# Optimization experiments

Hardware: AMD Instinct MI355X
Metric: run time of the kernel (lower is better)

## Reference

```python
import jax, jax.numpy as jnp
import numpy as np

B, T_MAX = 512, 200
FEAT, HID, MLP_HID, OUT = 256, 1024, 1024, 256


def _uniform(k, shape, fan_in):
    lim = 1.0 / np.sqrt(fan_in)
    return jax.random.uniform(k, shape, jnp.float32, -lim, lim)


def setup_inputs() -> dict:
    key = jax.random.key(0)
    ks = jax.random.split(key, 20)
    # lengths: sorted descending (packed-sequence convention), in [T_MAX//2, T_MAX]
    rng = np.random.RandomState(0)
    lengths = np.sort(rng.randint(T_MAX // 2, T_MAX + 1, size=B))[::-1].copy()
    inp = {
        "features": jax.random.normal(ks[0], (B, FEAT), jnp.float32),
        "lengths": jnp.asarray(lengths, jnp.int32),
        # pre-drawn reparameterization noise for the emission sampler, one per step
        "eps": jax.random.normal(ks[1], (T_MAX, B, OUT), jnp.float32),
        # feature2hidden Linear(feature_size, rnn_hidden_size)
        "W_f2h": _uniform(ks[2], (HID, FEAT), FEAT),
        "b_f2h": jnp.zeros((HID,), jnp.float32),
        # GRUCell(OUT, HID)
        "W_ih": _uniform(ks[3], (3 * HID, OUT), HID),
        "b_ih": _uniform(ks[4], (3 * HID,), HID),
        "W_hh": _uniform(ks[5], (3 * HID, HID), HID),
        "b_hh": _uniform(ks[6], (3 * HID,), HID),
        # MLP1 (emission param 1): Linear(HID, MLP_HID) -> tanh -> Linear(MLP_HID, OUT)
        "W1a": _uniform(ks[7], (MLP_HID, HID), HID), "b1a": jnp.zeros((MLP_HID,), jnp.float32),
        "W1b": _uniform(ks[8], (OUT, MLP_HID), MLP_HID), "b1b": jnp.zeros((OUT,), jnp.float32),
        # MLP2 (emission param 2)
        "W2a": _uniform(ks[9], (MLP_HID, HID), HID), "b2a": jnp.zeros((MLP_HID,), jnp.float32),
        "W2b": _uniform(ks[10], (OUT, MLP_HID), MLP_HID), "b2b": jnp.zeros((OUT,), jnp.float32),
        # offset_predictor Linear(HID, 2)  (computed then discarded in the original)
        "W_off": _uniform(ks[11], (2, HID), HID), "b_off": jnp.zeros((2,), jnp.float32),
    }
    return inp


def _packed_indices(lengths_np, T):
    # batch_sizes[t] = number of sequences with length > t (lengths sorted descending)
    bs = (lengths_np[None, :] > np.arange(T)[:, None]).sum(axis=1)
    t_idx = np.repeat(np.arange(T), bs)
    b_idx = np.concatenate([np.arange(b) for b in bs])
    return jnp.asarray(t_idx), jnp.asarray(b_idx)


def reference(features, lengths, eps, W_f2h, b_f2h, W_ih, b_ih, W_hh, b_hh,
              W1a, b1a, W1b, b1b, W2a, b2a, W2b, b2b, W_off, b_off):
    lengths_np = np.asarray(lengths)
    T = int(lengths_np.max())
    Bsz = features.shape[0]
    Dout = W_ih.shape[1]

    # (reshape_hidden returns None and init_hidden is never passed to the cell).
    _dead = features @ W_f2h.T + b_f2h

    gh_r, gh_z, gh_n = jnp.split(b_hh, 3)  # h_prev == 0 every step -> W_hh @ 0 drops out

    def mlp(h, Wa, ba, Wb, bb):
        return jnp.tanh(h @ Wa.T + ba) @ Wb.T + bb

    def step(x, eps_t):
        gi = x @ W_ih.T + b_ih                      # [B, 3H]
        gi_r, gi_z, gi_n = jnp.split(gi, 3, axis=-1)
        r = jax.nn.sigmoid(gi_r + gh_r)
        z = jax.nn.sigmoid(gi_z + gh_z)
        n = jnp.tanh(gi_n + r * gh_n)
        h = (1.0 - z) * n                           # GRUCell with zero init hidden
        p1 = mlp(h, W1a, b1a, W1b, b1b)             # emission param 1 (loc)
        p2 = mlp(h, W2a, b2a, W2b, b2b)             # emission param 2 (log-var)
        x_next = p1 + jnp.exp(0.5 * p2) * eps_t     # reparameterized Gaussian sample
        return x_next, (h, p1, p2)

    x0 = jnp.zeros((Bsz, Dout), features.dtype)
    _, (hs, p1s, p2s) = jax.lax.scan(step, x0, eps[:T])  # each [T, B, .]

    t_idx, b_idx = _packed_indices(lengths_np, T)
    flat_h = hs[t_idx, b_idx]     # [N, HID], N = sum(lengths)
    flat_p1 = p1s[t_idx, b_idx]   # [N, OUT]
    flat_p2 = p2s[t_idx, b_idx]   # [N, OUT]

    # offset predictor is computed but discarded by the original return statement
    _off = flat_h @ W_off.T + b_off

    return (flat_p1, flat_p2, flat_h)
```

## Files before the change

kernel.cpp:

```cpp
#include <hip/hip_runtime.h>
#include <math.h>

#define TMAX 200
#define CB   64

__device__ __forceinline__ float sig_(float x){ return 1.0f/(1.0f+expf(-x)); }

__device__ __forceinline__ void cl_sync(int* cnt, int* go, int nblk, int ep, int tid)
{
    __syncthreads();
    if (tid == 0) {
        __threadfence();
        int old = __hip_atomic_fetch_add(cnt, 1, __ATOMIC_ACQ_REL, __HIP_MEMORY_SCOPE_AGENT);
        if (old == nblk - 1) {
            __hip_atomic_store(cnt, 0, __ATOMIC_RELAXED, __HIP_MEMORY_SCOPE_AGENT);
            __hip_atomic_store(go, ep, __ATOMIC_RELEASE, __HIP_MEMORY_SCOPE_AGENT);
        } else {
            while (__hip_atomic_load(go, __ATOMIC_ACQUIRE, __HIP_MEMORY_SCOPE_AGENT) < ep)
                __builtin_amdgcn_s_sleep(16);
        }
        __threadfence();
    }
    __syncthreads();
}

#define LDSF 11264

__global__ __launch_bounds__(256, 2)
void kfused(const int* __restrict__ lengths,
            const float* __restrict__ eps,
            const float* __restrict__ W_ih, const float* __restrict__ b_ih,
            const float* __restrict__ b_hh,
            const float* __restrict__ W1a, const float* __restrict__ b1a,
            const float* __restrict__ W1b, const float* __restrict__ b1b,
            const float* __restrict__ W2a, const float* __restrict__ b2a,
            const float* __restrict__ W2b, const float* __restrict__ b2b,
            float* __restrict__ out_p1, float* __restrict__ out_p2, float* __restrict__ out_h,
            int* __restrict__ bar, float* __restrict__ xT, float* __restrict__ hT,
            float* __restrict__ haT, int nblk)
{
    __shared__ float lds[LDSF];
    __shared__ int sbs[TMAX], soff[TMAX];

    const int tid = threadIdx.x;
    const int bid = blockIdx.x;
    const int cl  = bid & 7;
    const int r   = bid >> 3;
    const int cb  = cl * CB;

    int* cnt = &bar[cl * 64];
    int* go  = &bar[cl * 64 + 16];

    if (tid < TMAX) {
        int c = 0;
        for (int b = 0; b < 512; ++b) c += (lengths[b] > tid) ? 1 : 0;
        sbs[tid] = c;
    }
    __syncthreads();
    if (tid == 0) { int a = 0; for (int i = 0; i < TMAX; ++i) { soff[i] = a; a += sbs[i]; } }
    __syncthreads();

    for (int t = 0; t < TMAX; ++t) {
        const int bsz = sbs[t], ofs = soff[t];

        for (int s = r; s < 32; s += nblk) {
            const int j0 = s * 32;
            const int tx = tid & 15, ty = tid >> 4;
            float acc[4][6];
            #pragma unroll
            for (int i = 0; i < 4; ++i)
                #pragma unroll
                for (int q = 0; q < 6; ++q) acc[i][q] = 0.f;

            if (t > 0) {
                const int sk = tid >> 3, sb = (tid & 7) * 8;
                const int wj = tid >> 3, wk = (tid & 7) * 4;
                float4 px0, px1, pw0, pw1, pw2;
                px0 = *(const float4*)&xT[(size_t)sk * 512 + cb + sb];
                px1 = *(const float4*)&xT[(size_t)sk * 512 + cb + sb + 4];
                pw0 = *(const float4*)&W_ih[(size_t)(j0 + wj) * 256 + wk];
                pw1 = *(const float4*)&W_ih[(size_t)(1024 + j0 + wj) * 256 + wk];
                pw2 = *(const float4*)&W_ih[(size_t)(2048 + j0 + wj) * 256 + wk];
                {
                    float* xs = lds; float* ws = lds + 4864;
                    *(float4*)&xs[sk * 76 + sb] = px0;
                    *(float4*)&xs[sk * 76 + sb + 4] = px1;
                    const float* a0 = &pw0.x; const float* a1 = &pw1.x; const float* a2 = &pw2.x;
                    #pragma unroll
                    for (int m = 0; m < 4; ++m) {
                        ws[(wk+m)*100 + wj]      = a0[m];
                        ws[(wk+m)*100 + 32 + wj] = a1[m];
                        ws[(wk+m)*100 + 64 + wj] = a2[m];
                    }
                }
                for (int kc = 0; kc < 8; ++kc) {
                    __syncthreads();
                    const int cur = kc & 1;
                    if (kc < 7) {
                        const int kb = (kc + 1) * 32;
                        px0 = *(const float4*)&xT[(size_t)(kb + sk) * 512 + cb + sb];
                        px1 = *(const float4*)&xT[(size_t)(kb + sk) * 512 + cb + sb + 4];
                        pw0 = *(const float4*)&W_ih[(size_t)(j0 + wj) * 256 + kb + wk];
                        pw1 = *(const float4*)&W_ih[(size_t)(1024 + j0 + wj) * 256 + kb + wk];
                        pw2 = *(const float4*)&W_ih[(size_t)(2048 + j0 + wj) * 256 + kb + wk];
                    }
                    const float* xs = lds + cur * 2432;
                    const float* ws = lds + 4864 + cur * 3200;
                    #pragma unroll 4
                    for (int kk = 0; kk < 32; ++kk) {
                        const float4 a4 = *(const float4*)&xs[kk * 76 + ty * 4];
                        float w[6];
                        #pragma unroll
                        for (int q = 0; q < 6; ++q) w[q] = ws[kk * 100 + tx * 6 + q];
                        const float av[4] = {a4.x, a4.y, a4.z, a4.w};
                        #pragma unroll
                        for (int i = 0; i < 4; ++i)
                            #pragma unroll
                            for (int q = 0; q < 6; ++q)
                                acc[i][q] = fmaf(av[i], w[q], acc[i][q]);
                    }
                    if (kc < 7) {
                        float* xs2 = lds + (cur ^ 1) * 2432;
                        float* ws2 = lds + 4864 + (cur ^ 1) * 3200;
                        *(float4*)&xs2[sk * 76 + sb] = px0;
                        *(float4*)&xs2[sk * 76 + sb + 4] = px1;
                        const float* a0 = &pw0.x; const float* a1 = &pw1.x; const float* a2 = &pw2.x;
                        #pragma unroll
                        for (int m = 0; m < 4; ++m) {
                            ws2[(wk+m)*100 + wj]      = a0[m];
                            ws2[(wk+m)*100 + 32 + wj] = a1[m];
                            ws2[(wk+m)*100 + 64 + wj] = a2[m];
                        }
                    }
                }
            }
            __syncthreads();
            #pragma unroll
            for (int q = 0; q < 6; ++q) {
                const int n = tx * 6 + q;
                #pragma unroll
                for (int i = 0; i < 4; ++i) lds[n * 68 + ty * 4 + i] = acc[i][q];
            }
            __syncthreads();
            {
                const int jr = tid & 31, bq = (tid >> 5) * 8;
                const int j = j0 + jr;
                const float brr = b_ih[j] + b_hh[j];
                const float bzz = b_ih[1024 + j] + b_hh[1024 + j];
                const float bnn = b_ih[2048 + j];
                const float gnn = b_hh[2048 + j];
                float hv[8];
                #pragma unroll
                for (int i = 0; i < 8; ++i) {
                    const int b = bq + i;
                    const float rr = sig_(lds[jr * 68 + b] + brr);
                    const float zz = sig_(lds[(32 + jr) * 68 + b] + bzz);
                    const float nn = tanhf(lds[(64 + jr) * 68 + b] + bnn + rr * gnn);
                    hv[i] = (1.f - zz) * nn;
                    hT[(size_t)j * 512 + cb + b] = hv[i];
                }
                #pragma unroll
                for (int i = 0; i < 8; ++i) lds[6528 + jr * 68 + bq + i] = hv[i];
            }
            __syncthreads();
            {
                const int b = tid >> 2, q = tid & 3;
                if (cb + b < bsz) {
                    float4 v0, v1;
                    v0.x = lds[6528 + (q*8+0)*68 + b]; v0.y = lds[6528 + (q*8+1)*68 + b];
                    v0.z = lds[6528 + (q*8+2)*68 + b]; v0.w = lds[6528 + (q*8+3)*68 + b];
                    v1.x = lds[6528 + (q*8+4)*68 + b]; v1.y = lds[6528 + (q*8+5)*68 + b];
                    v1.z = lds[6528 + (q*8+6)*68 + b]; v1.w = lds[6528 + (q*8+7)*68 + b];
                    *(float4*)&out_h[(size_t)(ofs + cb + b) * 1024 + j0 + q * 8] = v0;
                    *(float4*)&out_h[(size_t)(ofs + cb + b) * 1024 + j0 + q * 8 + 4] = v1;
                }
            }
            __syncthreads();
        }
        cl_sync(cnt, go, nblk, t * 3 + 1, tid);

        for (int s = r; s < 32; s += nblk) {
            const int n0 = s * 64;
            const float* __restrict__ Wa = (n0 < 1024) ? W1a : W2a;
            const float* __restrict__ ba = (n0 < 1024) ? b1a : b2a;
            const int nr0 = n0 & 1023;
            const int tx = tid & 15, ty = tid >> 4;
            const int sk = tid >> 3, sb = (tid & 7) * 8;
            const int wn = tid >> 2, wk0 = (tid & 3) * 8;
            float acc[4][4];
            #pragma unroll
            for (int i = 0; i < 4; ++i)
                #pragma unroll
                for (int j = 0; j < 4; ++j) acc[i][j] = 0.f;

            float4 px0, px1, pw0, pw1;
            px0 = *(const float4*)&hT[(size_t)sk * 512 + cb + sb];
            px1 = *(const float4*)&hT[(size_t)sk * 512 + cb + sb + 4];
            pw0 = *(const float4*)&Wa[(size_t)(nr0 + wn) * 1024 + wk0];
            pw1 = *(const float4*)&Wa[(size_t)(nr0 + wn) * 1024 + wk0 + 4];
            {
                float* xs = lds; float* ws = lds + 4864;
                *(float4*)&xs[sk * 76 + sb] = px0;
                *(float4*)&xs[sk * 76 + sb + 4] = px1;
                const float* a0 = &pw0.x; const float* a1 = &pw1.x;
                #pragma unroll
                for (int m = 0; m < 4; ++m) {
                    ws[(wk0+m)*68 + wn]   = a0[m];
                    ws[(wk0+4+m)*68 + wn] = a1[m];
                }
            }
            for (int kc = 0; kc < 32; ++kc) {
                __syncthreads();
                const int cur = kc & 1;
                if (kc < 31) {
                    const int kb = (kc + 1) * 32;
                    px0 = *(const float4*)&hT[(size_t)(kb + sk) * 512 + cb + sb];
                    px1 = *(const float4*)&hT[(size_t)(kb + sk) * 512 + cb + sb + 4];
                    pw0 = *(const float4*)&Wa[(size_t)(nr0 + wn) * 1024 + kb + wk0];
                    pw1 = *(const float4*)&Wa[(size_t)(nr0 + wn) * 1024 + kb + wk0 + 4];
                }
                const float* xs = lds + cur * 2432;
                const float* ws = lds + 4864 + cur * 3200;
                #pragma unroll 4
                for (int kk = 0; kk < 32; ++kk) {
                    const float4 a4 = *(const float4*)&xs[kk * 76 + ty * 4];
                    const float4 w4 = *(const float4*)&ws[kk * 68 + tx * 4];
                    const float av[4] = {a4.x, a4.y, a4.z, a4.w};
                    const float wv[4] = {w4.x, w4.y, w4.z, w4.w};
                    #pragma unroll
                    for (int i = 0; i < 4; ++i)
                        #pragma unroll
                        for (int j = 0; j < 4; ++j)
                            acc[i][j] = fmaf(av[i], wv[j], acc[i][j]);
                }
                if (kc < 31) {
                    float* xs2 = lds + (cur ^ 1) * 2432;
                    float* ws2 = lds + 4864 + (cur ^ 1) * 3200;
                    *(float4*)&xs2[sk * 76 + sb] = px0;
                    *(float4*)&xs2[sk * 76 + sb + 4] = px1;
                    const float* a0 = &pw0.x; const float* a1 = &pw1.x;
                    #pragma unroll
                    for (int m = 0; m < 4; ++m) {
                        ws2[(wk0+m)*68 + wn]   = a0[m];
                        ws2[(wk0+4+m)*68 + wn] = a1[m];
                    }
                }
            }
            #pragma unroll
            for (int j = 0; j < 4; ++j) {
                const float bias = ba[nr0 + tx * 4 + j];
                float4 hv;
                hv.x = tanhf(acc[0][j] + bias);
                hv.y = tanhf(acc[1][j] + bias);
                hv.z = tanhf(acc[2][j] + bias);
                hv.w = tanhf(acc[3][j] + bias);
                *(float4*)&haT[(size_t)(n0 + tx * 4 + j) * 512 + cb + ty * 4] = hv;
            }
            __syncthreads();
        }
        cl_sync(cnt, go, nblk, t * 3 + 2, tid);

        for (int s = r; s < 32; s += nblk) {
            const int c0 = s * 8;
            const int g = tid >> 6, b = tid & 63;
            const int sk = tid >> 3, sb = (tid & 7) * 8;
            float accf[2][8];
            #pragma unroll
            for (int f = 0; f < 2; ++f)
                #pragma unroll
                for (int c = 0; c < 8; ++c) accf[f][c] = 0.f;

            #pragma unroll 1
            for (int f = 0; f < 2; ++f) {
                const float* __restrict__ Wb = f ? W2b : W1b;
                const float* __restrict__ hap = haT + (size_t)f * 1024 * 512;
                float4 px0, px1, pwv;
                px0 = *(const float4*)&hap[(size_t)sk * 512 + cb + sb];
                px1 = *(const float4*)&hap[(size_t)sk * 512 + cb + sb + 4];
                const int cw = (tid & 63) >> 3, ck = (tid & 7) * 4;
                if (tid < 64) pwv = *(const float4*)&Wb[(size_t)(c0 + cw) * 1024 + ck];
                {
                    float* xs = lds; float* ws = lds + 4864;
                    *(float4*)&xs[sk * 76 + sb] = px0;
                    *(float4*)&xs[sk * 76 + sb + 4] = px1;
                    if (tid < 64) {
                        const float* a0 = &pwv.x;
                        #pragma unroll
                        for (int m = 0; m < 4; ++m) ws[(ck+m)*12 + cw] = a0[m];
                    }
                }
                for (int kc = 0; kc < 32; ++kc) {
                    __syncthreads();
                    const int cur = kc & 1;
                    if (kc < 31) {
                        const int kb = (kc + 1) * 32;
                        px0 = *(const float4*)&hap[(size_t)(kb + sk) * 512 + cb + sb];
                        px1 = *(const float4*)&hap[(size_t)(kb + sk) * 512 + cb + sb + 4];
                        if (tid < 64) pwv = *(const float4*)&Wb[(size_t)(c0 + cw) * 1024 + kb + ck];
                    }
                    const float* xs = lds + cur * 2432;
                    const float* ws = lds + 4864 + cur * 3200;
                    #pragma unroll
                    for (int k8 = 0; k8 < 8; ++k8) {
                        const int kk = g * 8 + k8;
                        const float a = xs[kk * 76 + b];
                        const float4 wlo = *(const float4*)&ws[kk * 12];
                        const float4 whi = *(const float4*)&ws[kk * 12 + 4];
                        accf[f][0] = fmaf(a, wlo.x, accf[f][0]);
                        accf[f][1] = fmaf(a, wlo.y, accf[f][1]);
                        accf[f][2] = fmaf(a, wlo.z, accf[f][2]);
                        accf[f][3] = fmaf(a, wlo.w, accf[f][3]);
                        accf[f][4] = fmaf(a, whi.x, accf[f][4]);
                        accf[f][5] = fmaf(a, whi.y, accf[f][5]);
                        accf[f][6] = fmaf(a, whi.z, accf[f][6]);
                        accf[f][7] = fmaf(a, whi.w, accf[f][7]);
                    }
                    if (kc < 31) {
                        float* xs2 = lds + (cur ^ 1) * 2432;
                        float* ws2 = lds + 4864 + (cur ^ 1) * 3200;
                        *(float4*)&xs2[sk * 76 + sb] = px0;
                        *(float4*)&xs2[sk * 76 + sb + 4] = px1;
                        if (tid < 64) {
                            const float* a0 = &pwv.x;
                            #pragma unroll
                            for (int m = 0; m < 4; ++m) ws2[(ck+m)*12 + cw] = a0[m];
                        }
                    }
                }
            }
            __syncthreads();
            #pragma unroll
            for (int c = 0; c < 8; ++c) {
                lds[((0 * 4 + g) * 8 + c) * 68 + b] = accf[0][c];
                lds[((1 * 4 + g) * 8 + c) * 68 + b] = accf[1][c];
            }
            {
                const int b2 = tid >> 2, q = tid & 3;
                const float2 e = *(const float2*)&eps[(size_t)t * 131072 + (size_t)(cb + b2) * 256 + c0 + q * 2];
                lds[4864 + b2 * 12 + q * 2]     = e.x;
                lds[4864 + b2 * 12 + q * 2 + 1] = e.y;
            }
            __syncthreads();
            {
                const int cp = tid >> 6;
                #pragma unroll
                for (int e = 0; e < 2; ++e) {
                    const int cc = cp * 2 + e;
                    float p1 = b1b[c0 + cc], p2 = b2b[c0 + cc];
                    #pragma unroll
                    for (int gg = 0; gg < 4; ++gg) {
                        p1 += lds[((0 * 4 + gg) * 8 + cc) * 68 + b];
                        p2 += lds[((1 * 4 + gg) * 8 + cc) * 68 + b];
                    }
                    const float x = fmaf(expf(0.5f * p2), lds[4864 + b * 12 + cc], p1);
                    xT[(size_t)(c0 + cc) * 512 + cb + b] = x;
                    lds[5700 + b * 20 + cc]     = p1;
                    lds[5700 + b * 20 + 8 + cc] = p2;
                }
            }
            __syncthreads();
            {
                const int bb2 = tid >> 2, q = tid & 3;
                if (cb + bb2 < bsz) {
                    if (q < 2) {
                        *(float4*)&out_p1[(size_t)(ofs + cb + bb2) * 256 + c0 + q * 4] =
                            *(const float4*)&lds[5700 + bb2 * 20 + q * 4];
                    } else {
                        *(float4*)&out_p2[(size_t)(ofs + cb + bb2) * 256 + c0 + (q - 2) * 4] =
                            *(const float4*)&lds[5700 + bb2 * 20 + 8 + (q - 2) * 4];
                    }
                }
            }
            __syncthreads();
        }
        cl_sync(cnt, go, nblk, t * 3 + 3, tid);
    }
}

extern "C" void kernel_launch(void* const* d_in, const int* in_sizes, int n_in,
                              void* d_out, int out_size, void* d_ws, size_t ws_size,
                              hipStream_t stream)
{
    (void)in_sizes; (void)n_in; (void)ws_size;
    const int*   lengths = (const int*)  d_in[1];
    const float* eps     = (const float*)d_in[2];
    const float* W_ih    = (const float*)d_in[5];
    const float* b_ih    = (const float*)d_in[6];
    const float* b_hh    = (const float*)d_in[8];
    const float* W1a     = (const float*)d_in[9];
    const float* b1a     = (const float*)d_in[10];
    const float* W1b     = (const float*)d_in[11];
    const float* b1b     = (const float*)d_in[12];
    const float* W2a     = (const float*)d_in[13];
    const float* b2a     = (const float*)d_in[14];
    const float* W2b     = (const float*)d_in[15];
    const float* b2b     = (const float*)d_in[16];

    float* out = (float*)d_out;
    const size_t N = (size_t)out_size / 1536;
    float* out_p1 = out;
    float* out_p2 = out + N * 256;
    float* out_h  = out + N * 512;

    int*   bar = (int*)d_ws;
    float* xT  = (float*)((char*)d_ws + 4096);
    float* hT  = xT + 131072;
    float* haT = hT + 524288;

    hipMemsetAsync(d_ws, 0, 4096, stream);

    int dev = 0;
    (void)hipGetDevice(&dev);
    int ncu = 0;
    if (hipDeviceGetAttribute(&ncu, hipDeviceAttributeMultiprocessorCount, dev) != hipSuccess || ncu <= 0)
        ncu = 256;
    int maxB = 0;
    if (hipOccupancyMaxActiveBlocksPerMultiprocessor(&maxB, (const void*)kfused, 256, 0) != hipSuccess || maxB <= 0)
        maxB = 1;
    long cap = (long)maxB * (long)ncu;
    int grd = (cap < 256) ? (int)(cap & ~7L) : 256;
    if (grd < 8) grd = 8;

    for (;;) {
        int nblk = grd >> 3;
        void* args[] = {
            (void*)&lengths, (void*)&eps, (void*)&W_ih, (void*)&b_ih, (void*)&b_hh,
            (void*)&W1a, (void*)&b1a, (void*)&W1b, (void*)&b1b,
            (void*)&W2a, (void*)&b2a, (void*)&W2b, (void*)&b2b,
            (void*)&out_p1, (void*)&out_p2, (void*)&out_h,
            (void*)&bar, (void*)&xT, (void*)&hT, (void*)&haT, (void*)&nblk
        };
        hipError_t err = hipLaunchCooperativeKernel((void*)kfused, dim3(grd), dim3(256), args, 0, stream);
        if (err == hipSuccess || grd <= 8) break;
        grd = (grd >> 1) & ~7;
        if (grd < 8) grd = 8;
    }
}
```

Measured before the change: 42.38 ms.

## Split batch into 16 clusters of 32 and shrink per-block tiles

Changes the cooperative decomposition from 8 batch clusters of 64 columns to 16 clusters of 32, doubling the grid to up to 512 blocks. Every GEMM tile, LDS layout and epilogue is rescaled to the 32-wide batch slice, and the MLP hidden stage is split into 64 tiles of 32 outputs. hT and haT writes are restaged through LDS so they go out as coalesced float4 stores. The aim is more blocks in flight per step and smaller per-cluster barrier groups. The cost is smaller register tiles with lower arithmetic intensity per LDS load, more blocks re-reading the weights, and the extra LDS staging passes.

```diff
diff --git a/kernel.cpp b/kernel.cpp
--- a/kernel.cpp
+++ b/kernel.cpp
@@ -2,7 +2,8 @@
 #include <math.h>
 
 #define TMAX 200
-#define CB   64
+#define NCL  16
+#define CB   32
 
 __device__ __forceinline__ float sig_(float x){ return 1.0f/(1.0f+expf(-x)); }
 
@@ -24,7 +25,7 @@
     __syncthreads();
 }
 
-#define LDSF 11264
+#define LDSF 8704
 
 __global__ __launch_bounds__(256, 2)
 void kfused(const int* __restrict__ lengths,
@@ -44,12 +45,12 @@
 
     const int tid = threadIdx.x;
     const int bid = blockIdx.x;
-    const int cl  = bid & 7;
-    const int r   = bid >> 3;
+    const int cl  = bid & 15;
+    const int r   = bid >> 4;
     const int cb  = cl * CB;
 
-    int* cnt = &bar[cl * 64];
-    int* go  = &bar[cl * 64 + 16];
+    int* cnt = &bar[cl * 16];
+    int* go  = &bar[cl * 16 + 8];
 
     if (tid < TMAX) {
         int c = 0;
@@ -66,25 +67,23 @@
         for (int s = r; s < 32; s += nblk) {
             const int j0 = s * 32;
             const int tx = tid & 15, ty = tid >> 4;
-            float acc[4][6];
+            float acc[2][6];
             #pragma unroll
-            for (int i = 0; i < 4; ++i)
+            for (int i = 0; i < 2; ++i)
                 #pragma unroll
                 for (int q = 0; q < 6; ++q) acc[i][q] = 0.f;
 
             if (t > 0) {
-                const int sk = tid >> 3, sb = (tid & 7) * 8;
+                const int sk = tid >> 3, sb = (tid & 7) * 4;
                 const int wj = tid >> 3, wk = (tid & 7) * 4;
-                float4 px0, px1, pw0, pw1, pw2;
-                px0 = *(const float4*)&xT[(size_t)sk * 512 + cb + sb];
-                px1 = *(const float4*)&xT[(size_t)sk * 512 + cb + sb + 4];
+                float4 px, pw0, pw1, pw2;
+                px  = *(const float4*)&xT[(size_t)sk * 512 + cb + sb];
                 pw0 = *(const float4*)&W_ih[(size_t)(j0 + wj) * 256 + wk];
                 pw1 = *(const float4*)&W_ih[(size_t)(1024 + j0 + wj) * 256 + wk];
                 pw2 = *(const float4*)&W_ih[(size_t)(2048 + j0 + wj) * 256 + wk];
                 {
-                    float* xs = lds; float* ws = lds + 4864;
-                    *(float4*)&xs[sk * 76 + sb] = px0;
-                    *(float4*)&xs[sk * 76 + sb + 4] = px1;
+                    float* xs = lds; float* ws = lds + 2304;
+                    *(float4*)&xs[sk * 36 + sb] = px;
                     const float* a0 = &pw0.x; const float* a1 = &pw1.x; const float* a2 = &pw2.x;
                     #pragma unroll
                     for (int m = 0; m < 4; ++m) {
@@ -98,32 +97,28 @@
                     const int cur = kc & 1;
                     if (kc < 7) {
                         const int kb = (kc + 1) * 32;
-                        px0 = *(const float4*)&xT[(size_t)(kb + sk) * 512 + cb + sb];
-                        px1 = *(const float4*)&xT[(size_t)(kb + sk) * 512 + cb + sb + 4];
+                        px  = *(const float4*)&xT[(size_t)(kb + sk) * 512 + cb + sb];
                         pw0 = *(const float4*)&W_ih[(size_t)(j0 + wj) * 256 + kb + wk];
                         pw1 = *(const float4*)&W_ih[(size_t)(1024 + j0 + wj) * 256 + kb + wk];
                         pw2 = *(const float4*)&W_ih[(size_t)(2048 + j0 + wj) * 256 + kb + wk];
                     }
-                    const float* xs = lds + cur * 2432;
-                    const float* ws = lds + 4864 + cur * 3200;
+                    const float* xs = lds + cur * 1152;
+                    const float* ws = lds + 2304 + cur * 3200;
                     #pragma unroll 4
                     for (int kk = 0; kk < 32; ++kk) {
-                        const float4 a4 = *(const float4*)&xs[kk * 76 + ty * 4];
-                        float w[6];
+                        const float a0v = xs[kk*36 + ty*2];
+                        const float a1v = xs[kk*36 + ty*2 + 1];
                         #pragma unroll
-                        for (int q = 0; q < 6; ++q) w[q] = ws[kk * 100 + tx * 6 + q];
-                        const float av[4] = {a4.x, a4.y, a4.z, a4.w};
-                        #pragma unroll
-                        for (int i = 0; i < 4; ++i)
-                            #pragma unroll
-                            for (int q = 0; q < 6; ++q)
-                                acc[i][q] = fmaf(av[i], w[q], acc[i][q]);
+                        for (int q = 0; q < 6; ++q) {
+                            const float w = ws[kk*100 + tx*6 + q];
+                            acc[0][q] = fmaf(a0v, w, acc[0][q]);
+                            acc[1][q] = fmaf(a1v, w, acc[1][q]);
+                        }
                     }
                     if (kc < 7) {
-                        float* xs2 = lds + (cur ^ 1) * 2432;
-                        float* ws2 = lds + 4864 + (cur ^ 1) * 3200;
-                        *(float4*)&xs2[sk * 76 + sb] = px0;
-                        *(float4*)&xs2[sk * 76 + sb + 4] = px1;
+                        float* xs2 = lds + (cur ^ 1) * 1152;
+                        float* ws2 = lds + 2304 + (cur ^ 1) * 3200;
+                        *(float4*)&xs2[sk * 36 + sb] = px;
                         const float* a0 = &pw0.x; const float* a1 = &pw1.x; const float* a2 = &pw2.x;
                         #pragma unroll
                         for (int m = 0; m < 4; ++m) {
@@ -138,123 +133,109 @@
             #pragma unroll
             for (int q = 0; q < 6; ++q) {
                 const int n = tx * 6 + q;
-                #pragma unroll
-                for (int i = 0; i < 4; ++i) lds[n * 68 + ty * 4 + i] = acc[i][q];
-            }
-            __syncthreads();
-            {
-                const int jr = tid & 31, bq = (tid >> 5) * 8;
+                lds[n*33 + ty*2]     = acc[0][q];
+                lds[n*33 + ty*2 + 1] = acc[1][q];
+            }
+            __syncthreads();
+            {
+                const int jr = tid & 31, bq = (tid >> 5) * 4;
                 const int j = j0 + jr;
                 const float brr = b_ih[j] + b_hh[j];
                 const float bzz = b_ih[1024 + j] + b_hh[1024 + j];
                 const float bnn = b_ih[2048 + j];
                 const float gnn = b_hh[2048 + j];
-                float hv[8];
-                #pragma unroll
-                for (int i = 0; i < 8; ++i) {
+                #pragma unroll
+                for (int i = 0; i < 4; ++i) {
                     const int b = bq + i;
-                    const float rr = sig_(lds[jr * 68 + b] + brr);
-                    const float zz = sig_(lds[(32 + jr) * 68 + b] + bzz);
-                    const float nn = tanhf(lds[(64 + jr) * 68 + b] + bnn + rr * gnn);
-                    hv[i] = (1.f - zz) * nn;
-                    hT[(size_t)j * 512 + cb + b] = hv[i];
-                }
-                #pragma unroll
-                for (int i = 0; i < 8; ++i) lds[6528 + jr * 68 + bq + i] = hv[i];
-            }
-            __syncthreads();
-            {
-                const int b = tid >> 2, q = tid & 3;
+                    const float rr = sig_(lds[jr*33 + b] + brr);
+                    const float zz = sig_(lds[(32+jr)*33 + b] + bzz);
+                    const float nn = tanhf(lds[(64+jr)*33 + b] + bnn + rr * gnn);
+                    lds[4096 + jr*33 + b] = (1.f - zz) * nn;
+                }
+            }
+            __syncthreads();
+            {
+                const int jj = tid >> 3, bq = (tid & 7) * 4;
+                float4 v = { lds[4096 + jj*33 + bq],     lds[4096 + jj*33 + bq + 1],
+                             lds[4096 + jj*33 + bq + 2], lds[4096 + jj*33 + bq + 3] };
+                *(float4*)&hT[(size_t)(j0 + jj) * 512 + cb + bq] = v;
+            }
+            {
+                const int b = tid >> 3, q = tid & 7;
                 if (cb + b < bsz) {
-                    float4 v0, v1;
-                    v0.x = lds[6528 + (q*8+0)*68 + b]; v0.y = lds[6528 + (q*8+1)*68 + b];
-                    v0.z = lds[6528 + (q*8+2)*68 + b]; v0.w = lds[6528 + (q*8+3)*68 + b];
-                    v1.x = lds[6528 + (q*8+4)*68 + b]; v1.y = lds[6528 + (q*8+5)*68 + b];
-                    v1.z = lds[6528 + (q*8+6)*68 + b]; v1.w = lds[6528 + (q*8+7)*68 + b];
-                    *(float4*)&out_h[(size_t)(ofs + cb + b) * 1024 + j0 + q * 8] = v0;
-                    *(float4*)&out_h[(size_t)(ofs + cb + b) * 1024 + j0 + q * 8 + 4] = v1;
+                    float4 v = { lds[4096 + (q*4+0)*33 + b], lds[4096 + (q*4+1)*33 + b],
+                                 lds[4096 + (q*4+2)*33 + b], lds[4096 + (q*4+3)*33 + b] };
+                    *(float4*)&out_h[(size_t)(ofs + cb + b) * 1024 + j0 + q*4] = v;
                 }
             }
             __syncthreads();
         }
         cl_sync(cnt, go, nblk, t * 3 + 1, tid);
 
-        for (int s = r; s < 32; s += nblk) {
-            const int n0 = s * 64;
+        for (int s = r; s < 64; s += nblk) {
+            const int n0 = s * 32;
             const float* __restrict__ Wa = (n0 < 1024) ? W1a : W2a;
             const float* __restrict__ ba = (n0 < 1024) ? b1a : b2a;
             const int nr0 = n0 & 1023;
             const int tx = tid & 15, ty = tid >> 4;
-            const int sk = tid >> 3, sb = (tid & 7) * 8;
-            const int wn = tid >> 2, wk0 = (tid & 3) * 8;
-            float acc[4][4];
-            #pragma unroll
-            for (int i = 0; i < 4; ++i)
-                #pragma unroll
-                for (int j = 0; j < 4; ++j) acc[i][j] = 0.f;
-
-            float4 px0, px1, pw0, pw1;
-            px0 = *(const float4*)&hT[(size_t)sk * 512 + cb + sb];
-            px1 = *(const float4*)&hT[(size_t)sk * 512 + cb + sb + 4];
-            pw0 = *(const float4*)&Wa[(size_t)(nr0 + wn) * 1024 + wk0];
-            pw1 = *(const float4*)&Wa[(size_t)(nr0 + wn) * 1024 + wk0 + 4];
-            {
-                float* xs = lds; float* ws = lds + 4864;
-                *(float4*)&xs[sk * 76 + sb] = px0;
-                *(float4*)&xs[sk * 76 + sb + 4] = px1;
-                const float* a0 = &pw0.x; const float* a1 = &pw1.x;
-                #pragma unroll
-                for (int m = 0; m < 4; ++m) {
-                    ws[(wk0+m)*68 + wn]   = a0[m];
-                    ws[(wk0+4+m)*68 + wn] = a1[m];
-                }
+            const int sk = tid >> 3, sb = (tid & 7) * 4;
+            const int wn = tid >> 3, wk0 = (tid & 7) * 4;
+            float acc[2][2] = {{0.f,0.f},{0.f,0.f}};
+
+            float4 px, pw;
+            px = *(const float4*)&hT[(size_t)sk * 512 + cb + sb];
+            pw = *(const float4*)&Wa[(size_t)(nr0 + wn) * 1024 + wk0];
+            {
+                float* xs = lds; float* ws = lds + 2304;
+                *(float4*)&xs[sk * 36 + sb] = px;
+                const float* a0 = &pw.x;
+                #pragma unroll
+                for (int m = 0; m < 4; ++m) ws[(wk0+m)*36 + wn] = a0[m];
             }
             for (int kc = 0; kc < 32; ++kc) {
                 __syncthreads();
                 const int cur = kc & 1;
                 if (kc < 31) {
                     const int kb = (kc + 1) * 32;
-                    px0 = *(const float4*)&hT[(size_t)(kb + sk) * 512 + cb + sb];
-                    px1 = *(const float4*)&hT[(size_t)(kb + sk) * 512 + cb + sb + 4];
-                    pw0 = *(const float4*)&Wa[(size_t)(nr0 + wn) * 1024 + kb + wk0];
-                    pw1 = *(const float4*)&Wa[(size_t)(nr0 + wn) * 1024 + kb + wk0 + 4];
-                }
-                const float* xs = lds + cur * 2432;
-                const float* ws = lds + 4864 + cur * 3200;
-                #pragma unroll 4
+                    px = *(const float4*)&hT[(size_t)(kb + sk) * 512 + cb + sb];
+                    pw = *(const float4*)&Wa[(size_t)(nr0 + wn) * 1024 + kb + wk0];
+                }
+                const float* xs = lds + cur * 1152;
+                const float* ws = lds + 2304 + cur * 1152;
+                #pragma unroll 8
                 for (int kk = 0; kk < 32; ++kk) {
-                    const float4 a4 = *(const float4*)&xs[kk * 76 + ty * 4];
-                    const float4 w4 = *(const float4*)&ws[kk * 68 + tx * 4];
-                    const float av[4] = {a4.x, a4.y, a4.z, a4.w};
-                    const float wv[4] = {w4.x, w4.y, w4.z, w4.w};
+                    const float a0v = xs[kk*36 + ty*2];
+                    const float a1v = xs[kk*36 + ty*2 + 1];
+                    const float w0 = ws[kk*36 + tx*2];
+                    const float w1 = ws[kk*36 + tx*2 + 1];
+                    acc[0][0] = fmaf(a0v, w0, acc[0][0]);
+                    acc[0][1] = fmaf(a0v, w1, acc[0][1]);
+                    acc[1][0] = fmaf(a1v, w0, acc[1][0]);
+                    acc[1][1] = fmaf(a1v, w1, acc[1][1]);
+                }
+                if (kc < 31) {
+                    float* xs2 = lds + (cur ^ 1) * 1152;
+                    float* ws2 = lds + 2304 + (cur ^ 1) * 1152;
+                    *(float4*)&xs2[sk * 36 + sb] = px;
+                    const float* a0 = &pw.x;
                     #pragma unroll
-                    for (int i = 0; i < 4; ++i)
-                        #pragma unroll
-                        for (int j = 0; j < 4; ++j)
-                            acc[i][j] = fmaf(av[i], wv[j], acc[i][j]);
-                }
-                if (kc < 31) {
-                    float* xs2 = lds + (cur ^ 1) * 2432;
-                    float* ws2 = lds + 4864 + (cur ^ 1) * 3200;
-                    *(float4*)&xs2[sk * 76 + sb] = px0;
-                    *(float4*)&xs2[sk * 76 + sb + 4] = px1;
-                    const float* a0 = &pw0.x; const float* a1 = &pw1.x;
-                    #pragma unroll
-                    for (int m = 0; m < 4; ++m) {
-                        ws2[(wk0+m)*68 + wn]   = a0[m];
-                        ws2[(wk0+4+m)*68 + wn] = a1[m];
-                    }
-                }
-            }
+                    for (int m = 0; m < 4; ++m) ws2[(wk0+m)*36 + wn] = a0[m];
+                }
+            }
+            __syncthreads();
             #pragma unroll
-            for (int j = 0; j < 4; ++j) {
-                const float bias = ba[nr0 + tx * 4 + j];
-                float4 hv;
-                hv.x = tanhf(acc[0][j] + bias);
-                hv.y = tanhf(acc[1][j] + bias);
-                hv.z = tanhf(acc[2][j] + bias);
-                hv.w = tanhf(acc[3][j] + bias);
-                *(float4*)&haT[(size_t)(n0 + tx * 4 + j) * 512 + cb + ty * 4] = hv;
+            for (int q = 0; q < 2; ++q) {
+                const int n = tx * 2 + q;
+                const float bias = ba[nr0 + n];
+                lds[n*33 + ty*2]     = tanhf(acc[0][q] + bias);
+                lds[n*33 + ty*2 + 1] = tanhf(acc[1][q] + bias);
+            }
+            __syncthreads();
+            {
+                const int nn = tid >> 3, bq = (tid & 7) * 4;
+                float4 v = { lds[nn*33 + bq],     lds[nn*33 + bq + 1],
+                             lds[nn*33 + bq + 2], lds[nn*33 + bq + 3] };
+                *(float4*)&haT[(size_t)(n0 + nn) * 512 + cb + bq] = v;
             }
             __syncthreads();
         }
@@ -262,8 +243,9 @@
 
         for (int s = r; s < 32; s += nblk) {
             const int c0 = s * 8;
-            const int g = tid >> 6, b = tid & 63;
-            const int sk = tid >> 3, sb = (tid & 7) * 8;
+            const int b = tid & 31, g = tid >> 5;
+            const int sk = tid >> 3, sb = (tid & 7) * 4;
+            const int cw = (tid & 63) >> 3, ck = (tid & 7) * 4;
             float accf[2][8];
             #pragma unroll
             for (int f = 0; f < 2; ++f)
@@ -274,17 +256,14 @@
             for (int f = 0; f < 2; ++f) {
                 const float* __restrict__ Wb = f ? W2b : W1b;
                 const float* __restrict__ hap = haT + (size_t)f * 1024 * 512;
-                float4 px0, px1, pwv;
-                px0 = *(const float4*)&hap[(size_t)sk * 512 + cb + sb];
-                px1 = *(const float4*)&hap[(size_t)sk * 512 + cb + sb + 4];
-                const int cw = (tid & 63) >> 3, ck = (tid & 7) * 4;
-                if (tid < 64) pwv = *(const float4*)&Wb[(size_t)(c0 + cw) * 1024 + ck];
+                float4 px, pw;
+                px = *(const float4*)&hap[(size_t)sk * 512 + cb + sb];
+                if (tid < 64) pw = *(const float4*)&Wb[(size_t)(c0 + cw) * 1024 + ck];
                 {
-                    float* xs = lds; float* ws = lds + 4864;
-                    *(float4*)&xs[sk * 76 + sb] = px0;
-                    *(float4*)&xs[sk * 76 + sb + 4] = px1;
+                    float* xs = lds; float* ws = lds + 2304;
+                    *(float4*)&xs[sk * 36 + sb] = px;
                     if (tid < 64) {
-                        const float* a0 = &pwv.x;
+                        const float* a0 = &pw.x;
                         #pragma unroll
                         for (int m = 0; m < 4; ++m) ws[(ck+m)*12 + cw] = a0[m];
                     }
@@ -294,18 +273,17 @@
                     const int cur = kc & 1;
                     if (kc < 31) {
                         const int kb = (kc + 1) * 32;
-                        px0 = *(const float4*)&hap[(size_t)(kb + sk) * 512 + cb + sb];
-                        px1 = *(const float4*)&hap[(size_t)(kb + sk) * 512 + cb + sb + 4];
-                        if (tid < 64) pwv = *(const float4*)&Wb[(size_t)(c0 + cw) * 1024 + kb + ck];
-                    }
-                    const float* xs = lds + cur * 2432;
-                    const float* ws = lds + 4864 + cur * 3200;
+                        px = *(const float4*)&hap[(size_t)(kb + sk) * 512 + cb + sb];
+                        if (tid < 64) pw = *(const float4*)&Wb[(size_t)(c0 + cw) * 1024 + kb + ck];
+                    }
+                    const float* xs = lds + cur * 1152;
+                    const float* ws = lds + 2304 + cur * 384;
                     #pragma unroll
-                    for (int k8 = 0; k8 < 8; ++k8) {
-                        const int kk = g * 8 + k8;
-                        const float a = xs[kk * 76 + b];
-                        const float4 wlo = *(const float4*)&ws[kk * 12];
-                        const float4 whi = *(const float4*)&ws[kk * 12 + 4];
+                    for (int kq = 0; kq < 4; ++kq) {
+                        const int kk = g * 4 + kq;
+                        const float a = xs[kk*36 + b];
+                        const float4 wlo = *(const float4*)&ws[kk*12];
+                        const float4 whi = *(const float4*)&ws[kk*12 + 4];
                         accf[f][0] = fmaf(a, wlo.x, accf[f][0]);
                         accf[f][1] = fmaf(a, wlo.y, accf[f][1]);
                         accf[f][2] = fmaf(a, wlo.z, accf[f][2]);
@@ -316,59 +294,44 @@
                         accf[f][7] = fmaf(a, whi.w, accf[f][7]);
                     }
                     if (kc < 31) {
-                        float* xs2 = lds + (cur ^ 1) * 2432;
-                        float* ws2 = lds + 4864 + (cur ^ 1) * 3200;
-                        *(float4*)&xs2[sk * 76 + sb] = px0;
-                        *(float4*)&xs2[sk * 76 + sb + 4] = px1;
+                        float* xs2 = lds + (cur ^ 1) * 1152;
+                        float* ws2 = lds + 2304 + (cur ^ 1) * 384;
+                        *(float4*)&xs2[sk * 36 + sb] = px;
                         if (tid < 64) {
-                            const float* a0 = &pwv.x;
+                            const float* a0 = &pw.x;
                             #pragma unroll
                             for (int m = 0; m < 4; ++m) ws2[(ck+m)*12 + cw] = a0[m];
                         }
                     }
                 }
-            }
-            __syncthreads();
-            #pragma unroll
-            for (int c = 0; c < 8; ++c) {
-                lds[((0 * 4 + g) * 8 + c) * 68 + b] = accf[0][c];
-                lds[((1 * 4 + g) * 8 + c) * 68 + b] = accf[1][c];
-            }
-            {
-                const int b2 = tid >> 2, q = tid & 3;
-                const float2 e = *(const float2*)&eps[(size_t)t * 131072 + (size_t)(cb + b2) * 256 + c0 + q * 2];
-                lds[4864 + b2 * 12 + q * 2]     = e.x;
-                lds[4864 + b2 * 12 + q * 2 + 1] = e.y;
-            }
-            __syncthreads();
-            {
-                const int cp = tid >> 6;
-                #pragma unroll
-                for (int e = 0; e < 2; ++e) {
-                    const int cc = cp * 2 + e;
-                    float p1 = b1b[c0 + cc], p2 = b2b[c0 + cc];
-                    #pragma unroll
-                    for (int gg = 0; gg < 4; ++gg) {
-                        p1 += lds[((0 * 4 + gg) * 8 + cc) * 68 + b];
-                        p2 += lds[((1 * 4 + gg) * 8 + cc) * 68 + b];
-                    }
-                    const float x = fmaf(expf(0.5f * p2), lds[4864 + b * 12 + cc], p1);
-                    xT[(size_t)(c0 + cc) * 512 + cb + b] = x;
-                    lds[5700 + b * 20 + cc]     = p1;
-                    lds[5700 + b * 20 + 8 + cc] = p2;
-                }
-            }
-            __syncthreads();
-            {
-                const int bb2 = tid >> 2, q = tid & 3;
-                if (cb + bb2 < bsz) {
-                    if (q < 2) {
-                        *(float4*)&out_p1[(size_t)(ofs + cb + bb2) * 256 + c0 + q * 4] =
-                            *(const float4*)&lds[5700 + bb2 * 20 + q * 4];
-                    } else {
-                        *(float4*)&out_p2[(size_t)(ofs + cb + bb2) * 256 + c0 + (q - 2) * 4] =
-                            *(const float4*)&lds[5700 + bb2 * 20 + 8 + (q - 2) * 4];
-                    }
+                #pragma unroll
+                for (int c = 0; c < 8; ++c)
+                    lds[3072 + ((f*8 + g)*8 + c)*33 + b] = accf[f][c];
+                __syncthreads();
+            }
+            {
+                const int cc = tid >> 5, bb = tid & 31;
+                float p1 = b1b[c0 + cc], p2 = b2b[c0 + cc];
+                #pragma unroll
+                for (int g2 = 0; g2 < 8; ++g2) {
+                    p1 += lds[3072 + ((0*8 + g2)*8 + cc)*33 + bb];
+                    p2 += lds[3072 + ((1*8 + g2)*8 + cc)*33 + bb];
+                }
+                const float e = eps[(size_t)t * 131072 + (size_t)(cb + bb) * 256 + c0 + cc];
+                xT[(size_t)(c0 + cc) * 512 + cb + bb] = fmaf(expf(0.5f * p2), e, p1);
+                lds[7296 + bb*24 + cc]     = p1;
+                lds[7296 + bb*24 + 8 + cc] = p2;
+            }
+            __syncthreads();
+            {
+                const int bb = tid >> 3, q = tid & 7;
+                if (cb + bb < bsz) {
+                    if (q < 2)
+                        *(float4*)&out_p1[(size_t)(ofs + cb + bb) * 256 + c0 + q*4] =
+                            *(const float4*)&lds[7296 + bb*24 + q*4];
+                    else if (q < 4)
+                        *(float4*)&out_p2[(size_t)(ofs + cb + bb) * 256 + c0 + (q-2)*4] =
+                            *(const float4*)&lds[7296 + bb*24 + 8 + (q-2)*4];
                 }
             }
             __syncthreads();
@@ -418,11 +381,11 @@
     if (hipOccupancyMaxActiveBlocksPerMultiprocessor(&maxB, (const void*)kfused, 256, 0) != hipSuccess || maxB <= 0)
         maxB = 1;
     long cap = (long)maxB * (long)ncu;
-    int grd = (cap < 256) ? (int)(cap & ~7L) : 256;
-    if (grd < 8) grd = 8;
+    int grd = (cap < 512) ? (int)(cap & ~15L) : 512;
+    if (grd < 16) grd = 16;
 
     for (;;) {
-        int nblk = grd >> 3;
+        int nblk = grd >> 4;
         void* args[] = {
             (void*)&lengths, (void*)&eps, (void*)&W_ih, (void*)&b_ih, (void*)&b_hh,
             (void*)&W1a, (void*)&b1a, (void*)&W1b, (void*)&b1b,
@@ -431,8 +394,8 @@
             (void*)&bar, (void*)&xT, (void*)&hT, (void*)&haT, (void*)&nblk
         };
         hipError_t err = hipLaunchCooperativeKernel((void*)kfused, dim3(grd), dim3(256), args, 0, stream);
-        if (err == hipSuccess || grd <= 8) break;
-        grd = (grd >> 1) & ~7;
-        if (grd < 8) grd = 8;
+        if (err == hipSuccess || grd <= 16) break;
+        grd = (grd >> 1) & ~15;
+        if (grd < 16) grd = 16;
     }
 }
```

Measured after the change: 60.30 ms. 42.3% more time.
